# Kernel tuning notes

Measured on AMD Instinct MI355X. Metric: run time of the kernel, lower is better.

## Reference

```python
import jax, jax.numpy as jnp
import numpy as np

B, S, H = 4, 2048, 2048
NH, NKV, HD = 16, 4, 128  # heads, kv heads, head_dim; group g = NH // NKV = 4
ROPE_BASE = 10000.0


def rotate_half(x):
    x1, x2 = jnp.split(x, 2, axis=-1)
    return jnp.concatenate([-x2, x1], axis=-1)


def setup_inputs() -> dict:
    key = jax.random.key(0)
    k1, k2, k3 = jax.random.split(key, 3)
    hidden_states = jax.random.normal(k1, (B, S, H), dtype=jnp.float32)
    # additive causal mask [B, 1, S, S]: 0 on/below diagonal, large negative above
    causal = jnp.tril(jnp.ones((S, S), dtype=bool))
    attention_mask = jnp.where(causal, 0.0, -1e9).astype(jnp.float32)
    attention_mask = jnp.broadcast_to(attention_mask[None, None], (B, 1, S, S))
    # RoPE tables [S, HD]
    inv_freq = 1.0 / (ROPE_BASE ** (np.arange(0, HD, 2, dtype=np.float32) / HD))
    pos = np.arange(S, dtype=np.float32)
    freqs = np.outer(pos, inv_freq)                       # [S, HD/2]
    emb = np.concatenate([freqs, freqs], axis=-1)         # [S, HD]
    rope_cos = jnp.asarray(np.cos(emb), dtype=jnp.float32)
    rope_sin = jnp.asarray(np.sin(emb), dtype=jnp.float32)
    w_attn = jax.random.normal(k2, (H, H + 2 * NKV * HD), dtype=jnp.float32) * 0.02
    w_proj = jax.random.normal(k3, (H, H), dtype=jnp.float32) * 0.02
    return {"hidden_states": hidden_states, "attention_mask": attention_mask,
            "rope_cos": rope_cos, "rope_sin": rope_sin,
            "w_attn": w_attn, "w_proj": w_proj}


def reference(hidden_states, attention_mask, rope_cos, rope_sin, w_attn, w_proj):
    g = NH // NKV
    qkv = jnp.einsum('bsh,hf->bsf', hidden_states, w_attn)          # [B,S,(g+2)*NKV*HD]
    qkv = qkv.reshape(B, S, NKV, (g + 2) * HD)
    q, k, v = jnp.split(qkv, [g * HD, (g + 1) * HD], axis=-1)
    q = q.reshape(B, S, NH, HD).transpose(0, 2, 1, 3)               # [B,NH,S,HD]
    k = k.transpose(0, 2, 1, 3)                                     # [B,NKV,S,HD]
    v = v.transpose(0, 2, 1, 3)                                     # [B,NKV,S,HD]
    cos = rope_cos[None, None]                                      # [1,1,S,HD]
    sin = rope_sin[None, None]
    q = q * cos + rotate_half(q) * sin
    k = k * cos + rotate_half(k) * sin
    # repeat kv heads to match query heads (repeat_interleave semantics)
    k = jnp.repeat(k, g, axis=1)                                    # [B,NH,S,HD]
    v = jnp.repeat(v, g, axis=1)
    scale = 1.0 / (HD ** 0.5)
    scores = jnp.einsum('bhqd,bhkd->bhqk', q, k) * scale + attention_mask
    attn = jax.nn.softmax(scores.astype(jnp.float32), axis=-1).astype(q.dtype)
    out = jnp.einsum('bhqk,bhkd->bhqd', attn, v)                    # [B,NH,S,HD]
    out = out.transpose(0, 2, 1, 3).reshape(B, S, NH * HD)
    return jnp.einsum('bsh,hf->bsf', out, w_proj)
```

## Files before the change

### kernel.cpp

```cpp
#include <hip/hip_runtime.h>
#include <hip/hip_bf16.h>
#include <stdint.h>

#define B_   4
#define S_   2048
#define H_   2048
#define NH_  16
#define NKV_ 4
#define HD_  128
#define F_   3072

typedef __bf16 bf16x8 __attribute__((ext_vector_type(8)));
typedef float  f32x4  __attribute__((ext_vector_type(4)));
typedef unsigned short u16;

#define GLOAD_LDS16(gp, lp)                                                             \
  __builtin_amdgcn_global_load_lds((const __attribute__((address_space(1))) void*)(gp), \
                                   (__attribute__((address_space(3))) void*)(lp), 16, 0, 0)

__device__ __forceinline__ u16 f2bf(float f) {
  union { float f; uint32_t u; } v; v.f = f;
  uint32_t r = (v.u + 0x7FFFu + ((v.u >> 16) & 1u)) >> 16;
  return (u16)r;
}
__device__ __forceinline__ float bf2f(u16 u) {
  union { uint32_t u; float f; } v; v.u = ((uint32_t)u) << 16;
  return v.f;
}

__global__ void k_cvt_bf16(const float* __restrict__ in, u16* __restrict__ out, int n4) {
  int i = blockIdx.x * 256 + threadIdx.x;
  if (i >= n4) return;
  float4 v = ((const float4*)in)[i];
  union { u16 s[4]; uint2 u; } o;
  o.s[0] = f2bf(v.x); o.s[1] = f2bf(v.y); o.s[2] = f2bf(v.z); o.s[3] = f2bf(v.w);
  ((uint2*)out)[i] = o.u;
}

__global__ void k_transpose_cvt(const float* __restrict__ in, u16* __restrict__ out, int R, int C) {
  __shared__ u16 tile[64][68];
  int c0 = blockIdx.x * 64, r0 = blockIdx.y * 64;
  int t = threadIdx.x;
#pragma unroll
  for (int j = 0; j < 16; ++j) {
    int e = j * 256 + t;
    int r = e >> 6, c = e & 63;
    tile[r][c] = f2bf(in[(size_t)(r0 + r) * C + (c0 + c)]);
  }
  __syncthreads();
#pragma unroll
  for (int j = 0; j < 16; ++j) {
    int e = j * 256 + t;
    int c = e >> 6, r = e & 63;
    out[(size_t)(c0 + c) * R + (r0 + r)] = tile[r][c];
  }
}

template <bool OUTF32>
__global__ __launch_bounds__(256) void k_gemm_bt(const u16* __restrict__ A, const u16* __restrict__ BT,
                                                 void* __restrict__ Cv, int M, int N, int K) {
  __shared__ u16 lA[2][128 * 64];
  __shared__ u16 lB[2][128 * 64];
  int t = threadIdx.x, w = t >> 6, l = t & 63, c = l & 15, g = l >> 4;
  int bn = blockIdx.x * 128, bm = blockIdx.y * 128;
  int wm = (w >> 1) * 64, wn = (w & 1) * 64;

  f32x4 acc[4][4];
#pragma unroll
  for (int mi = 0; mi < 4; ++mi)
#pragma unroll
    for (int ni = 0; ni < 4; ++ni) acc[mi][ni] = (f32x4){0.f, 0.f, 0.f, 0.f};

  int nk = K >> 6;
  int srow = l >> 3;
  int scol = ((l & 7) ^ srow) * 8;

#define GEMM_STAGE(k0, buf)                                                     \
  _Pragma("unroll")                                                             \
  for (int i = 0; i < 4; ++i) {                                                 \
    int ch = i * 4 + w; int row = ch * 8 + srow;                                \
    GLOAD_LDS16(&A [(size_t)(bm + row) * K + (k0) + scol], &lA[buf][ch * 512]); \
    GLOAD_LDS16(&BT[(size_t)(bn + row) * K + (k0) + scol], &lB[buf][ch * 512]); \
  }

  GEMM_STAGE(0, 0)
  asm volatile("s_waitcnt vmcnt(0)" ::: "memory");
  __syncthreads();
  int cur = 0;
  for (int kt = 0; kt < nk; ++kt) {
    if (kt + 1 < nk) { GEMM_STAGE((kt + 1) << 6, cur ^ 1) }
    const u16* cA = lA[cur];
    const u16* cB = lB[cur];
#pragma unroll
    for (int s = 0; s < 2; ++s) {
      bf16x8 af[4], bfr[4];
#pragma unroll
      for (int mi = 0; mi < 4; ++mi) {
        int row = wm + mi * 16 + c;
        af[mi] = *(const bf16x8*)&cA[row * 64 + (((s * 4 + g) ^ (c & 7)) * 8)];
      }
#pragma unroll
      for (int ni = 0; ni < 4; ++ni) {
        int row = wn + ni * 16 + c;
        bfr[ni] = *(const bf16x8*)&cB[row * 64 + (((s * 4 + g) ^ (c & 7)) * 8)];
      }
#pragma unroll
      for (int mi = 0; mi < 4; ++mi)
#pragma unroll
        for (int ni = 0; ni < 4; ++ni)
          acc[mi][ni] = __builtin_amdgcn_mfma_f32_16x16x32_bf16(af[mi], bfr[ni], acc[mi][ni], 0, 0, 0);
    }
    if (kt + 1 < nk) {
      asm volatile("s_waitcnt vmcnt(0)" ::: "memory");
      __syncthreads();
      cur ^= 1;
    }
  }
#pragma unroll
  for (int mi = 0; mi < 4; ++mi)
#pragma unroll
    for (int ni = 0; ni < 4; ++ni)
#pragma unroll
      for (int r = 0; r < 4; ++r) {
        size_t row = (size_t)bm + wm + mi * 16 + 4 * g + r;
        size_t col = (size_t)bn + wn + ni * 16 + c;
        if constexpr (OUTF32) ((float*)Cv)[row * N + col] = acc[mi][ni][r];
        else                  ((u16*)Cv)  [row * N + col] = f2bf(acc[mi][ni][r]);
      }
#undef GEMM_STAGE
}

__global__ void k_rope_qk(const u16* __restrict__ qkv, const float* __restrict__ ct,
                          const float* __restrict__ st, u16* __restrict__ Q, u16* __restrict__ Kd) {
  size_t idx = (size_t)blockIdx.x * 256 + threadIdx.x;
  const size_t NQ = (size_t)B_ * NH_ * S_ * HD_;
  int d, s, row, col; size_t oidx; u16* dst;
  if (idx < NQ) {
    d = (int)(idx & 127); s = (int)((idx >> 7) & (S_ - 1));
    int h = (int)((idx >> 18) & 15); int b = (int)(idx >> 22);
    row = b * S_ + s;
    col = (h >> 2) * 768 + (h & 3) * 128 + d;
    dst = Q; oidx = idx;
  } else {
    size_t i2 = idx - NQ;
    d = (int)(i2 & 127); s = (int)((i2 >> 7) & (S_ - 1));
    int kvh = (int)((i2 >> 18) & 3); int b = (int)(i2 >> 20);
    row = b * S_ + s;
    col = kvh * 768 + 512 + d;
    dst = Kd; oidx = i2;
  }
  float x  = bf2f(qkv[(size_t)row * F_ + col]);
  float xr = (d < 64) ? -bf2f(qkv[(size_t)row * F_ + col + 64])
                      :  bf2f(qkv[(size_t)row * F_ + col - 64]);
  float o = x * ct[s * HD_ + d] + xr * st[s * HD_ + d];
  dst[oidx] = f2bf(o);
}

__global__ void k_transpose_v(const u16* __restrict__ qkv, u16* __restrict__ Vt) {
  __shared__ u16 tile[64][136];
  int s0 = blockIdx.x * 64;
  int b = blockIdx.y >> 2, kvh = blockIdx.y & 3;
  int t = threadIdx.x;
  const u16* src = qkv + (size_t)(b * S_ + s0) * F_ + kvh * 768 + 640;
#pragma unroll
  for (int j = 0; j < 4; ++j) {
    int e = j * 256 + t;
    int sl = e >> 4, ch = e & 15;
    *(uint4*)&tile[sl][ch * 8] = *(const uint4*)&src[(size_t)sl * F_ + ch * 8];
  }
  __syncthreads();
  u16* dstb = Vt + (size_t)(b * NKV_ + kvh) * HD_ * S_;
#pragma unroll
  for (int j = 0; j < 4; ++j) {
    int e = j * 256 + t;
    int d = e & 127, sc = e >> 7;
    u16 tmp[8];
#pragma unroll
    for (int i = 0; i < 8; ++i) tmp[i] = tile[sc * 8 + i][d];
    *(uint4*)&dstb[(size_t)d * S_ + s0 + sc * 8] = *(const uint4*)tmp;
  }
}

__global__ __launch_bounds__(512, 4) void k_flash(const u16* __restrict__ Q, const u16* __restrict__ K,
                                                  const u16* __restrict__ Vt, u16* __restrict__ O) {
  __shared__ u16 lK[2][64 * 128];
  __shared__ u16 lV[2][128 * 64];
  __shared__ u16 lP[8][16 * 64];
  int t = threadIdx.x, w = t >> 6, l = t & 63, c = l & 15, g = l >> 4;
  int qb = (int)(gridDim.x - 1 - blockIdx.x);
  int bh = blockIdx.y;
  int b = bh >> 4, h = bh & 15, kvh = h >> 2;
  int qw = qb * 128 + w * 16;
  const u16* Qb = Q  + (size_t)(b * NH_  + h)   * S_ * HD_;
  const u16* Kb = K  + (size_t)(b * NKV_ + kvh) * S_ * HD_;
  const u16* Vb = Vt + (size_t)(b * NKV_ + kvh) * HD_ * S_;

  bf16x8 qf[4];
#pragma unroll
  for (int sl = 0; sl < 4; ++sl)
    qf[sl] = *(const bf16x8*)&Qb[(size_t)(qw + c) * HD_ + sl * 32 + g * 8];

  f32x4 oacc[8];
#pragma unroll
  for (int nd = 0; nd < 8; ++nd) oacc[nd] = (f32x4){0.f, 0.f, 0.f, 0.f};
  float m_run = -1e30f, l_run = 0.f;

  int ntiles = 2 * qb + 2;
  int krl = l >> 4;
  int vrl = l >> 3;

#define STAGE_KV(kv0, buf)                                                           \
  _Pragma("unroll")                                                                  \
  for (int i = 0; i < 2; ++i) {                                                      \
    int ch = i * 8 + w;                                                              \
    int rrK = ch * 4 + krl;                                                          \
    int jK  = (l & 15) ^ (rrK & 15);                                                 \
    GLOAD_LDS16(&Kb[(size_t)((kv0) + rrK) * HD_ + jK * 8], &lK[buf][ch * 512]);      \
    int rdV = ch * 8 + vrl;                                                          \
    int jV  = (l & 7) ^ (rdV & 7);                                                   \
    GLOAD_LDS16(&Vb[(size_t)rdV * S_ + (kv0) + jV * 8], &lV[buf][ch * 512]);         \
  }

  STAGE_KV(0, 0)
  asm volatile("s_waitcnt vmcnt(0)" ::: "memory");
  __syncthreads();
  int cur = 0;

  for (int kt = 0; kt < ntiles; ++kt) {
    int kv0 = kt * 64;
    if (kt + 1 < ntiles) { STAGE_KV(kv0 + 64, cur ^ 1) }
    const u16* cK = lK[cur];
    const u16* cV = lV[cur];
    if (kv0 <= qw + 15) {
      f32x4 sc[4];
#pragma unroll
      for (int f = 0; f < 4; ++f) sc[f] = (f32x4){0.f, 0.f, 0.f, 0.f};
#pragma unroll
      for (int sl = 0; sl < 4; ++sl)
#pragma unroll
        for (int f = 0; f < 4; ++f) {
          bf16x8 kf = *(const bf16x8*)&cK[(f * 16 + c) * 128 + (((sl * 4 + g) ^ c) * 8)];
          sc[f] = __builtin_amdgcn_mfma_f32_16x16x32_bf16(kf, qf[sl], sc[f], 0, 0, 0);
        }
      const float SCL = 0.088388347648318447f * 1.4426950408889634f;
      bool partial = (kv0 + 63 > qw);
      float pvv[4][4];
      float pm = -1e30f;
#pragma unroll
      for (int f = 0; f < 4; ++f)
#pragma unroll
        for (int r = 0; r < 4; ++r) {
          float v = sc[f][r] * SCL;
          if (partial && (kv0 + f * 16 + 4 * g + r > qw + c)) v = -1e30f;
          pvv[f][r] = v;
          pm = fmaxf(pm, v);
        }
      pm = fmaxf(pm, __shfl_xor(pm, 16));
      pm = fmaxf(pm, __shfl_xor(pm, 32));
      if (!__all(pm - m_run <= 8.0f)) {
        float m_new = fmaxf(m_run, pm);
        float alpha = exp2f(m_run - m_new);
        l_run *= alpha;
#pragma unroll
        for (int r = 0; r < 4; ++r) {
          float ar = __shfl(alpha, 4 * g + r);
#pragma unroll
          for (int nd = 0; nd < 8; ++nd) oacc[nd][r] *= ar;
        }
        m_run = m_new;
      }
      float ps = 0.f;
#pragma unroll
      for (int f = 0; f < 4; ++f)
#pragma unroll
        for (int r = 0; r < 4; ++r) {
          float p = exp2f(pvv[f][r] - m_run);
          pvv[f][r] = p;
          ps += p;
        }
      ps += __shfl_xor(ps, 16);
      ps += __shfl_xor(ps, 32);
      l_run += ps;
      char* Pw = (char*)&lP[w][0];
#pragma unroll
      for (int f = 0; f < 4; ++f) {
        int base = f * 32 + g * 8;
        int chunk = base >> 4, within = base & 15;
        uint32_t p01 = (uint32_t)f2bf(pvv[f][0]) | ((uint32_t)f2bf(pvv[f][1]) << 16);
        uint32_t p23 = (uint32_t)f2bf(pvv[f][2]) | ((uint32_t)f2bf(pvv[f][3]) << 16);
        int rowb = c * 128 + ((chunk ^ (c & 7)) << 4) + within;
        *(uint32_t*)(Pw + rowb)     = p01;
        *(uint32_t*)(Pw + rowb + 4) = p23;
      }
#pragma unroll
      for (int ks = 0; ks < 2; ++ks) {
        bf16x8 pf = *(const bf16x8*)(Pw + c * 128 + (((ks * 4 + g) ^ (c & 7)) << 4));
#pragma unroll
        for (int nd = 0; nd < 8; ++nd) {
          int rowv = nd * 16 + c;
          bf16x8 vf = *(const bf16x8*)&cV[rowv * 64 + (((ks * 4 + g) ^ (c & 7)) * 8)];
          oacc[nd] = __builtin_amdgcn_mfma_f32_16x16x32_bf16(pf, vf, oacc[nd], 0, 0, 0);
        }
      }
    }
    if (kt + 1 < ntiles) {
      asm volatile("s_waitcnt vmcnt(0)" ::: "memory");
      __syncthreads();
      cur ^= 1;
    }
  }
#undef STAGE_KV
  float lr[4];
#pragma unroll
  for (int r = 0; r < 4; ++r) {
    float lv = __shfl(l_run, 4 * g + r);
    lr[r] = 1.f / lv;
  }
#pragma unroll
  for (int nd = 0; nd < 8; ++nd)
#pragma unroll
    for (int r = 0; r < 4; ++r) {
      size_t row = (size_t)b * S_ + (qw + 4 * g + r);
      O[row * (NH_ * HD_) + h * HD_ + nd * 16 + c] = f2bf(oacc[nd][r] * lr[r]);
    }
}

extern "C" void kernel_launch(void* const* d_in, const int* in_sizes, int n_in,
                              void* d_out, int out_size, void* d_ws, size_t ws_size,
                              hipStream_t stream) {
  const float* hid   = (const float*)d_in[0];
  const float* rcos  = (const float*)d_in[2];
  const float* rsin  = (const float*)d_in[3];
  const float* wattn = (const float*)d_in[4];
  const float* wproj = (const float*)d_in[5];

  u16* ws   = (u16*)d_ws;
  u16* hidB = ws;
  u16* wAT  = ws + 16777216;
  u16* wPT  = ws + 23068672;
  u16* qkv  = ws + 27262976;
  u16* Qs   = ws + 52428800;
  u16* Ks   = ws + 69206016;
  u16* Vts  = ws + 73400320;
  u16* Os   = qkv;

  k_cvt_bf16<<<16384, 256, 0, stream>>>(hid, hidB, 16777216 / 4);
  k_transpose_cvt<<<dim3(48, 32), 256, 0, stream>>>(wattn, wAT, 2048, 3072);
  k_transpose_cvt<<<dim3(32, 32), 256, 0, stream>>>(wproj, wPT, 2048, 2048);
  k_gemm_bt<false><<<dim3(24, 64), 256, 0, stream>>>(hidB, wAT, qkv, 8192, 3072, 2048);
  k_rope_qk<<<81920, 256, 0, stream>>>(qkv, rcos, rsin, Qs, Ks);
  k_transpose_v<<<dim3(32, 16), 256, 0, stream>>>(qkv, Vts);
  k_flash<<<dim3(16, 64), 512, 0, stream>>>(Qs, Ks, Vts, Os);
  k_gemm_bt<true><<<dim3(16, 64), 256, 0, stream>>>(Os, wPT, d_out, 8192, 2048, 2048);
}
```

Before: 605.1 us.

## Replace 128x128 GEMM with 256x256 tiled, deeper-prefetch, XCD-swizzled kernel

```diff
diff --git a/kernel.cpp b/kernel.cpp
--- a/kernel.cpp
+++ b/kernel.cpp
@@ -57,67 +57,91 @@
 }
 
 template <bool OUTF32>
-__global__ __launch_bounds__(256) void k_gemm_bt(const u16* __restrict__ A, const u16* __restrict__ BT,
-                                                 void* __restrict__ Cv, int M, int N, int K) {
-  __shared__ u16 lA[2][128 * 64];
-  __shared__ u16 lB[2][128 * 64];
+__global__ __launch_bounds__(512, 2) void k_gemm256(const u16* __restrict__ A, const u16* __restrict__ BT,
+                                                    void* __restrict__ Cv, int M, int N, int K) {
+  __shared__ u16 lA[2][256 * 64];
+  __shared__ u16 lB[2][256 * 64];
   int t = threadIdx.x, w = t >> 6, l = t & 63, c = l & 15, g = l >> 4;
-  int bn = blockIdx.x * 128, bm = blockIdx.y * 128;
-  int wm = (w >> 1) * 64, wn = (w & 1) * 64;
-
-  f32x4 acc[4][4];
-#pragma unroll
-  for (int mi = 0; mi < 4; ++mi)
+  int gx = gridDim.x, nwg = gx * gridDim.y;
+  int lin = blockIdx.y * gx + blockIdx.x;
+  int swz = (lin & 7) * (nwg >> 3) + (lin >> 3);
+  int bn = (swz % gx) * 256, bm = (swz / gx) * 256;
+  int wm = (w >> 2) * 128, wn = (w & 3) * 64;
+
+  f32x4 acc[8][4];
+#pragma unroll
+  for (int mi = 0; mi < 8; ++mi)
 #pragma unroll
     for (int ni = 0; ni < 4; ++ni) acc[mi][ni] = (f32x4){0.f, 0.f, 0.f, 0.f};
 
-  int nk = K >> 6;
   int srow = l >> 3;
-  int scol = ((l & 7) ^ srow) * 8;
-
-#define GEMM_STAGE(k0, buf)                                                     \
-  _Pragma("unroll")                                                             \
-  for (int i = 0; i < 4; ++i) {                                                 \
-    int ch = i * 4 + w; int row = ch * 8 + srow;                                \
-    GLOAD_LDS16(&A [(size_t)(bm + row) * K + (k0) + scol], &lA[buf][ch * 512]); \
-    GLOAD_LDS16(&BT[(size_t)(bn + row) * K + (k0) + scol], &lB[buf][ch * 512]); \
-  }
-
-  GEMM_STAGE(0, 0)
-  asm volatile("s_waitcnt vmcnt(0)" ::: "memory");
-  __syncthreads();
-  int cur = 0;
-  for (int kt = 0; kt < nk; ++kt) {
-    if (kt + 1 < nk) { GEMM_STAGE((kt + 1) << 6, cur ^ 1) }
-    const u16* cA = lA[cur];
-    const u16* cB = lB[cur];
-#pragma unroll
-    for (int s = 0; s < 2; ++s) {
-      bf16x8 af[4], bfr[4];
-#pragma unroll
-      for (int mi = 0; mi < 4; ++mi) {
-        int row = wm + mi * 16 + c;
-        af[mi] = *(const bf16x8*)&cA[row * 64 + (((s * 4 + g) ^ (c & 7)) * 8)];
-      }
-#pragma unroll
-      for (int ni = 0; ni < 4; ++ni) {
+  int sj   = ((l & 7) ^ srow) * 8;
+
+#define STG(s_, buf_)                                                                          \
+  _Pragma("unroll")                                                                            \
+  for (int gld = 0; gld < 4; ++gld) {                                                          \
+    int ch = gld * 8 + w;                                                                      \
+    GLOAD_LDS16(&A [(size_t)(bm + ch * 8 + srow) * K + ((s_) << 6) + sj], &lA[buf_][ch * 512]);\
+    GLOAD_LDS16(&BT[(size_t)(bn + ch * 8 + srow) * K + ((s_) << 6) + sj], &lB[buf_][ch * 512]);\
+  }
+
+#define CLUSTER(mh, nh)                                                                        \
+  __builtin_amdgcn_s_setprio(1);                                                               \
+  _Pragma("unroll")                                                                            \
+  for (int mi2 = 0; mi2 < 4; ++mi2)                                                            \
+    _Pragma("unroll")                                                                          \
+    for (int ni2 = 0; ni2 < 2; ++ni2)                                                          \
+      _Pragma("unroll")                                                                        \
+      for (int kk = 0; kk < 2; ++kk)                                                           \
+        acc[(mh) * 4 + mi2][(nh) * 2 + ni2] = __builtin_amdgcn_mfma_f32_16x16x32_bf16(         \
+            af[mi2][kk], bfr[(nh) * 2 + ni2][kk], acc[(mh) * 4 + mi2][(nh) * 2 + ni2], 0, 0, 0);\
+  __builtin_amdgcn_s_setprio(0);                                                               \
+  __builtin_amdgcn_s_barrier();
+
+  STG(0, 0)
+  STG(1, 1)
+  int nst = K >> 6;
+  for (int s = 0; s < nst; ++s) {
+    int buf = s & 1;
+    if (s == nst - 1) { asm volatile("s_waitcnt vmcnt(0)" ::: "memory"); }
+    else              { asm volatile("s_waitcnt vmcnt(8)" ::: "memory"); }
+    __builtin_amdgcn_s_barrier();
+    const u16* cA = lA[buf];
+    const u16* cB = lB[buf];
+    bf16x8 af[4][2], bfr[4][2];
+#pragma unroll
+    for (int mi2 = 0; mi2 < 4; ++mi2)
+#pragma unroll
+      for (int kk = 0; kk < 2; ++kk) {
+        int row = wm + mi2 * 16 + c;
+        af[mi2][kk] = *(const bf16x8*)&cA[row * 64 + (((kk * 4 + g) ^ (c & 7)) * 8)];
+      }
+#pragma unroll
+    for (int ni = 0; ni < 4; ++ni)
+#pragma unroll
+      for (int kk = 0; kk < 2; ++kk) {
         int row = wn + ni * 16 + c;
-        bfr[ni] = *(const bf16x8*)&cB[row * 64 + (((s * 4 + g) ^ (c & 7)) * 8)];
-      }
-#pragma unroll
-      for (int mi = 0; mi < 4; ++mi)
-#pragma unroll
-        for (int ni = 0; ni < 4; ++ni)
-          acc[mi][ni] = __builtin_amdgcn_mfma_f32_16x16x32_bf16(af[mi], bfr[ni], acc[mi][ni], 0, 0, 0);
-    }
-    if (kt + 1 < nk) {
-      asm volatile("s_waitcnt vmcnt(0)" ::: "memory");
-      __syncthreads();
-      cur ^= 1;
-    }
-  }
-#pragma unroll
-  for (int mi = 0; mi < 4; ++mi)
+        bfr[ni][kk] = *(const bf16x8*)&cB[row * 64 + (((kk * 4 + g) ^ (c & 7)) * 8)];
+      }
+    __builtin_amdgcn_s_barrier();
+    CLUSTER(0, 0)
+    CLUSTER(0, 1)
+#pragma unroll
+    for (int mi2 = 0; mi2 < 4; ++mi2)
+#pragma unroll
+      for (int kk = 0; kk < 2; ++kk) {
+        int row = wm + 64 + mi2 * 16 + c;
+        af[mi2][kk] = *(const bf16x8*)&cA[row * 64 + (((kk * 4 + g) ^ (c & 7)) * 8)];
+      }
+    __builtin_amdgcn_s_barrier();
+    CLUSTER(1, 0)
+    if (s + 2 < nst) { STG(s + 2, buf) }
+    CLUSTER(1, 1)
+  }
+#undef STG
+#undef CLUSTER
+#pragma unroll
+  for (int mi = 0; mi < 8; ++mi)
 #pragma unroll
     for (int ni = 0; ni < 4; ++ni)
 #pragma unroll
@@ -127,7 +151,6 @@
         if constexpr (OUTF32) ((float*)Cv)[row * N + col] = acc[mi][ni][r];
         else                  ((u16*)Cv)  [row * N + col] = f2bf(acc[mi][ni][r]);
       }
-#undef GEMM_STAGE
 }
 
 __global__ void k_rope_qk(const u16* __restrict__ qkv, const float* __restrict__ ct,
@@ -347,9 +370,9 @@
   k_cvt_bf16<<<16384, 256, 0, stream>>>(hid, hidB, 16777216 / 4);
   k_transpose_cvt<<<dim3(48, 32), 256, 0, stream>>>(wattn, wAT, 2048, 3072);
   k_transpose_cvt<<<dim3(32, 32), 256, 0, stream>>>(wproj, wPT, 2048, 2048);
-  k_gemm_bt<false><<<dim3(24, 64), 256, 0, stream>>>(hidB, wAT, qkv, 8192, 3072, 2048);
+  k_gemm256<false><<<dim3(12, 32), 512, 0, stream>>>(hidB, wAT, qkv, 8192, 3072, 2048);
   k_rope_qk<<<81920, 256, 0, stream>>>(qkv, rcos, rsin, Qs, Ks);
   k_transpose_v<<<dim3(32, 16), 256, 0, stream>>>(qkv, Vts);
   k_flash<<<dim3(16, 64), 512, 0, stream>>>(Qs, Ks, Vts, Os);
-  k_gemm_bt<true><<<dim3(16, 64), 256, 0, stream>>>(Os, wPT, d_out, 8192, 2048, 2048);
-}
+  k_gemm256<true><<<dim3(8, 32), 512, 0, stream>>>(Os, wPT, d_out, 8192, 2048, 2048);
+}
```

Result: slower. 620.2 us (+2.5%).
